# Kernel tuning notes

Measured on AMD Instinct MI355X. Metric: run time of the kernel, lower is better.

## Reference

```python
import jax, jax.numpy as jnp
import numpy as np

B, T, E, HD = 8, 2048, 1024, 64  # batch, seq (== n_ctx), n_embd, head_dim = n_embd // n_head


def setup_inputs() -> dict:
    key = jax.random.key(0)
    k1, k2, k3, k4 = jax.random.split(key, 4)
    x = jax.random.normal(k1, (B, T, E), dtype=jnp.float32)
    s = E ** -0.5  # Linear-like init scale
    Wq = jax.random.normal(k2, (E, HD), dtype=jnp.float32) * s
    Wk = jax.random.normal(k3, (E, HD), dtype=jnp.float32) * s
    Wv = jax.random.normal(k4, (E, HD), dtype=jnp.float32) * s
    return {"x": x, "Wq": Wq, "Wk": Wk, "Wv": Wv}


def reference(x, Wq, Wk, Wv):
    # q,k,v: [B, T, HD]
    q = jnp.einsum('bte,eh->bth', x, Wq)
    k = jnp.einsum('bte,eh->bth', x, Wk)
    v = jnp.einsum('bte,eh->bth', x, Wv)
    scale = k.shape[-1] ** -0.5
    # scores: [B, T, T]
    alpha = jnp.einsum('bqh,bkh->bqk', q, k) * scale
    causal = jnp.tril(jnp.ones((T, T), dtype=bool))
    alpha = jnp.where(causal, alpha, -jnp.inf)
    alpha = jax.nn.softmax(alpha, axis=-1)
    # dropout with p=0.0 is identity in eval
    h = jnp.einsum('bqk,bkh->bqh', alpha, v)  # [B, T, HD]
    return h
```

## Files before the change

### kernel.cpp

```cpp
#include <hip/hip_runtime.h>
#include <hip/hip_bf16.h>
#include <math.h>

#define BATCH 8
#define T 2048
#define E 1024
#define HD 64
#define BT (BATCH * T)

typedef __bf16 bf16_t;
typedef bf16_t bf16x4 __attribute__((ext_vector_type(4)));
typedef bf16_t bf16x8 __attribute__((ext_vector_type(8)));
typedef float f32x4 __attribute__((ext_vector_type(4)));

#define MFMA(a, b, c) __builtin_amdgcn_mfma_f32_16x16x32_bf16((a), (b), (c), 0, 0, 0)

#define QSCALE (0.125f * 1.44269504088896340736f)


__global__ __launch_bounds__(256) void prep_w(const float* __restrict__ Wq,
                                              const float* __restrict__ Wk,
                                              const float* __restrict__ Wv,
                                              bf16_t* __restrict__ WTt) {
    const int nt  = blockIdx.x >> 3;
    const int kc0 = (blockIdx.x & 7) * 128;
    const int tid = threadIdx.x;
    const int l16 = tid & 15;
    const int k8  = (kc0 >> 3) + (tid >> 4);
    const int n   = nt * 16 + l16;
    const int m   = n >> 6;
    const int col = n & 63;
    const float* W = (m == 0) ? Wq : (m == 1) ? Wk : Wv;
    const float scale = (m == 0) ? QSCALE : 1.0f;
    bf16x8 o;
#pragma unroll
    for (int j = 0; j < 8; j++) {
        o[j] = (bf16_t)(W[(size_t)(k8 * 8 + j) * HD + col] * scale);
    }
    *reinterpret_cast<bf16x8*>(WTt + (size_t)nt * 16384 + k8 * 128 + l16 * 8) = o;
}

__global__ __launch_bounds__(512, 2) void qkv_proj(
    const float* __restrict__ x,
    const bf16_t* __restrict__ WTt,
    bf16_t* __restrict__ qt,
    bf16_t* __restrict__ kt,
    bf16_t* __restrict__ vt)
{
    __shared__ __align__(16) bf16_t xb[64][1024];

    const int tid  = threadIdx.x;
    const int lane = tid & 63;
    const int l16  = lane & 15;
    const int quad = lane >> 4;
    const int wc   = (tid >> 6) & 3;
    const int wr   = tid >> 8;
    const int rowbase0 = blockIdx.x * 64;

    {
        const int r   = tid >> 3;
        const int s   = tid & 7;
        const int swz = (r & 7) << 4;
        const float* gsrc = x + (size_t)(rowbase0 + r) * E + s * 128;
        char* drow = reinterpret_cast<char*>(&xb[r][0]);
#pragma unroll
        for (int half = 0; half < 2; half++) {
            f32x4 v[16];
#pragma unroll
            for (int i = 0; i < 16; i++)
                v[i] = *reinterpret_cast<const f32x4*>(gsrc + half * 64 + i * 4);
            __builtin_amdgcn_sched_barrier(0);
#pragma unroll
            for (int j = 0; j < 8; j++) {
                bf16x8 w8;
#pragma unroll
                for (int u = 0; u < 4; u++) {
                    w8[u]     = (bf16_t)v[2 * j][u];
                    w8[4 + u] = (bf16_t)v[2 * j + 1][u];
                }
                const int off = s * 256 + half * 128 + j * 16;
                *reinterpret_cast<bf16x8*>(drow + (off ^ swz)) = w8;
            }
        }
    }
    __syncthreads();

    const bf16_t* Bb = WTt + (size_t)(wc * 3) * 16384 + lane * 8;
    f32x4 acc[2][3] = {};

    for (int kc = 0; kc < E; kc += 64) {
        bf16x8 bf[2][3];
#pragma unroll
        for (int ks = 0; ks < 2; ks++)
#pragma unroll
            for (int tc = 0; tc < 3; tc++)
                bf[ks][tc] = *reinterpret_cast<const bf16x8*>(
                    Bb + (size_t)tc * 16384 + (kc + ks * 32) * 16);

#pragma unroll
        for (int g = 0; g < 2; g++) {
            const int row = wr * 32 + g * 16 + l16;
            const int swz = (row & 7) << 4;
            const char* rbase = reinterpret_cast<const char*>(&xb[row][0]);
            const bf16x8 a0 = *reinterpret_cast<const bf16x8*>(
                rbase + ((kc * 2 + quad * 16) ^ swz));
            const bf16x8 a1 = *reinterpret_cast<const bf16x8*>(
                rbase + ((kc * 2 + 64 + quad * 16) ^ swz));
#pragma unroll
            for (int tc = 0; tc < 3; tc++) acc[g][tc] = MFMA(a0, bf[0][tc], acc[g][tc]);
#pragma unroll
            for (int tc = 0; tc < 3; tc++) acc[g][tc] = MFMA(a1, bf[1][tc], acc[g][tc]);
        }
    }

#pragma unroll
    for (int g = 0; g < 2; g++) {
        const int rowbase = rowbase0 + wr * 32 + g * 16;
#pragma unroll
        for (int tc = 0; tc < 3; tc++) {
            const int n0  = wc * 48 + tc * 16;
            const int m   = n0 >> 6;
            const int tcg = (n0 & 63) >> 4;
            if (m < 2) {
                bf16_t* dst = (m == 0) ? qt : kt;
                const size_t o0 = (size_t)(rowbase >> 4) * 1024 +
                                  (size_t)(tcg * 2 + (l16 >> 3)) * 128 + (l16 & 7);
#pragma unroll
                for (int r = 0; r < 4; r++) {
                    dst[o0 + (quad * 4 + r) * 8] = (bf16_t)acc[g][tc][r];
                }
            } else {
                const int b_    = rowbase >> 11;
                const int tbase = rowbase & (T - 1);
                const size_t o0 = (size_t)b_ * 131072 +
                                  (size_t)((tbase >> 3) + (quad >> 1)) * 128 +
                                  l16 * 8 + (quad & 1) * 4 + (size_t)tcg * 32768;
                bf16x4 pv;
#pragma unroll
                for (int r = 0; r < 4; r++) pv[r] = (bf16_t)acc[g][tc][r];
                *reinterpret_cast<bf16x4*>(vt + o0) = pv;
            }
        }
    }
}

__global__ __launch_bounds__(512, 2) void attn(
    const bf16_t* __restrict__ qtl,
    const bf16_t* __restrict__ ktl,
    const bf16_t* __restrict__ vtl,
    float* __restrict__ out)
{
    __shared__ __align__(16) bf16_t plds[8][16][40];
    __shared__ float opart[8][16][66];
    __shared__ float lpart[8][16];

    const int wave = threadIdx.x >> 6;
    const int lane = threadIdx.x & 63;
    const int l16  = lane & 15;
    const int quad = lane >> 4;
    const int group = wave >> 2;
    const int kw    = wave & 3;

    const int b  = blockIdx.x >> 6;
    const int pr = blockIdx.x & 63;
    const int qt = group ? (127 - pr) : pr;
    const int rowbase = qt * 16;

    const bf16_t* Qb = qtl + (size_t)((b * T + rowbase) >> 4) * 1024 + lane * 8;
    const bf16_t* Kb = ktl + (size_t)b * T * 64 + lane * 8;
    const bf16_t* Vb = vtl + (size_t)b * 131072 + lane * 8;

    const bf16x8 qf0 = *reinterpret_cast<const bf16x8*>(Qb);
    const bf16x8 qf1 = *reinterpret_cast<const bf16x8*>(Qb + 512);

    f32x4 o[4] = {};
    f32x4 lrun = {};

    const int nch = (rowbase + 47) >> 5;

    int k0 = kw * 32;
    bf16x8 kfa0 = *reinterpret_cast<const bf16x8*>(Kb + k0 * 64);
    bf16x8 kfb0 = *reinterpret_cast<const bf16x8*>(Kb + k0 * 64 + 512);
    bf16x8 kfa1 = *reinterpret_cast<const bf16x8*>(Kb + k0 * 64 + 1024);
    bf16x8 kfb1 = *reinterpret_cast<const bf16x8*>(Kb + k0 * 64 + 1536);
    bf16x8 vf0 = *reinterpret_cast<const bf16x8*>(Vb + k0 * 16);
    bf16x8 vf1 = *reinterpret_cast<const bf16x8*>(Vb + k0 * 16 + 32768);
    bf16x8 vf2 = *reinterpret_cast<const bf16x8*>(Vb + k0 * 16 + 65536);
    bf16x8 vf3 = *reinterpret_cast<const bf16x8*>(Vb + k0 * 16 + 98304);

    for (int c = kw; c < nch; c += 4) {
        k0 = c * 32;
        const int cn = (c + 4 < nch) ? (c + 4) : c;
        const int kn = cn * 32;
        bf16x8 nkfa0 = *reinterpret_cast<const bf16x8*>(Kb + kn * 64);
        bf16x8 nkfb0 = *reinterpret_cast<const bf16x8*>(Kb + kn * 64 + 512);
        bf16x8 nkfa1 = *reinterpret_cast<const bf16x8*>(Kb + kn * 64 + 1024);
        bf16x8 nkfb1 = *reinterpret_cast<const bf16x8*>(Kb + kn * 64 + 1536);
        bf16x8 nvf0 = *reinterpret_cast<const bf16x8*>(Vb + kn * 16);
        bf16x8 nvf1 = *reinterpret_cast<const bf16x8*>(Vb + kn * 16 + 32768);
        bf16x8 nvf2 = *reinterpret_cast<const bf16x8*>(Vb + kn * 16 + 65536);
        bf16x8 nvf3 = *reinterpret_cast<const bf16x8*>(Vb + kn * 16 + 98304);

        f32x4 s_lo = {};
        f32x4 s_hi = {};
        s_lo = MFMA(qf0, kfa0, s_lo);
        s_lo = MFMA(qf1, kfb0, s_lo);
        s_hi = MFMA(qf0, kfa1, s_hi);
        s_hi = MFMA(qf1, kfb1, s_hi);

        if (k0 + 31 > rowbase) {
            const int row = rowbase + quad * 4;
#pragma unroll
            for (int r = 0; r < 4; r++) {
                if (k0 + l16 > row + r)      s_lo[r] = -INFINITY;
                if (k0 + 16 + l16 > row + r) s_hi[r] = -INFINITY;
            }
        }

#pragma unroll
        for (int r = 0; r < 4; r++) {
            const float p0 = exp2f(s_lo[r]);
            const float p1 = exp2f(s_hi[r]);
            lrun[r] += p0 + p1;
            plds[wave][quad * 4 + r][l16]      = (bf16_t)p0;
            plds[wave][quad * 4 + r][16 + l16] = (bf16_t)p1;
        }
        const bf16x8 pf = *reinterpret_cast<const bf16x8*>(&plds[wave][l16][quad * 8]);

        o[0] = MFMA(pf, vf0, o[0]);
        o[1] = MFMA(pf, vf1, o[1]);
        o[2] = MFMA(pf, vf2, o[2]);
        o[3] = MFMA(pf, vf3, o[3]);

        kfa0 = nkfa0; kfb0 = nkfb0; kfa1 = nkfa1; kfb1 = nkfb1;
        vf0 = nvf0; vf1 = nvf1; vf2 = nvf2; vf3 = nvf3;
    }

#pragma unroll
    for (int r = 0; r < 4; r++) {
        float l = lrun[r];
        l += __shfl_xor(l, 1);
        l += __shfl_xor(l, 2);
        l += __shfl_xor(l, 4);
        l += __shfl_xor(l, 8);
        if (l16 == 0) lpart[wave][quad * 4 + r] = l;
#pragma unroll
        for (int nb = 0; nb < 4; nb++) {
            opart[wave][quad * 4 + r][nb * 16 + l16] = o[nb][r];
        }
    }
    __syncthreads();

    const int g    = threadIdx.x >> 8;
    const int gtid = threadIdx.x & 255;
    const int qtg  = g ? (127 - pr) : pr;
    const size_t outbase = (size_t)b * T + qtg * 16;
#pragma unroll
    for (int pass = 0; pass < 4; pass++) {
        const int row = pass * 4 + (gtid >> 6);
        const int col = gtid & 63;
        float osum = 0.f, lsum = 0.f;
#pragma unroll
        for (int w = 0; w < 4; w++) {
            osum += opart[g * 4 + w][row][col];
            lsum += lpart[g * 4 + w][row];
        }
        out[(outbase + row) * HD + col] = osum / lsum;
    }
}

extern "C" void kernel_launch(void* const* d_in, const int* in_sizes, int n_in,
                              void* d_out, int out_size, void* d_ws, size_t ws_size,
                              hipStream_t stream) {
    const float* x  = (const float*)d_in[0];
    const float* Wq = (const float*)d_in[1];
    const float* Wk = (const float*)d_in[2];
    const float* Wv = (const float*)d_in[3];
    float* out = (float*)d_out;

    bf16_t* ws  = (bf16_t*)d_ws;
    bf16_t* WTt = ws;
    bf16_t* qtl = WTt + (size_t)192 * E;
    bf16_t* ktl = qtl + (size_t)BT * HD;
    bf16_t* vtl = ktl + (size_t)BT * HD;

    prep_w<<<96, 256, 0, stream>>>(Wq, Wk, Wv, WTt);
    qkv_proj<<<256, 512, 0, stream>>>(x, WTt, qtl, ktl, vtl);
    attn<<<512, 512, 0, stream>>>(qtl, ktl, vtl, out);
}
```

Baseline: 122.9 us.

## Split QKV projection K dimension across wave halves with LDS reduction

The QKV projection kernel now gives each wave all 64 rows and half of the K dimension, rather than half of the rows and all of K. Partial accumulators from the second wave group are reduced through shared memory (reusing the x buffer) before the first group writes output. This halves the weight-fragment global loads per wave relative to MFMA work. The x staging load is also reorganised so a wave's lanes read contiguous 1 KB segments, for more coalesced global reads. In exchange it adds two extra barriers, an LDS partial-sum round trip, and more accumulator registers per wave.

Measured after the change: 119.4 us. -2.9%, faster.

```diff
diff --git a/kernel.cpp b/kernel.cpp
--- a/kernel.cpp
+++ b/kernel.cpp
@@ -50,62 +50,65 @@
     __shared__ __align__(16) bf16_t xb[64][1024];
 
     const int tid  = threadIdx.x;
+    const int w    = tid >> 6;
     const int lane = tid & 63;
     const int l16  = lane & 15;
     const int quad = lane >> 4;
-    const int wc   = (tid >> 6) & 3;
-    const int wr   = tid >> 8;
+    const int wk   = w >> 2;
+    const int wc   = w & 3;
     const int rowbase0 = blockIdx.x * 64;
 
     {
-        const int r   = tid >> 3;
-        const int s   = tid & 7;
-        const int swz = (r & 7) << 4;
-        const float* gsrc = x + (size_t)(rowbase0 + r) * E + s * 128;
-        char* drow = reinterpret_cast<char*>(&xb[r][0]);
-#pragma unroll
-        for (int half = 0; half < 2; half++) {
-            f32x4 v[16];
-#pragma unroll
-            for (int i = 0; i < 16; i++)
-                v[i] = *reinterpret_cast<const f32x4*>(gsrc + half * 64 + i * 4);
+#pragma unroll
+        for (int rd = 0; rd < 4; rd++) {
+            f32x4 v[8];
+#pragma unroll
+            for (int j = 0; j < 8; j++) {
+                const int gi = w * 32 + rd * 8 + j;
+                const int r  = gi >> 2;
+                const int q  = gi & 3;
+                v[j] = *reinterpret_cast<const f32x4*>(
+                    x + (size_t)(rowbase0 + r) * E + q * 256 + lane * 4);
+            }
             __builtin_amdgcn_sched_barrier(0);
 #pragma unroll
             for (int j = 0; j < 8; j++) {
-                bf16x8 w8;
-#pragma unroll
-                for (int u = 0; u < 4; u++) {
-                    w8[u]     = (bf16_t)v[2 * j][u];
-                    w8[4 + u] = (bf16_t)v[2 * j + 1][u];
-                }
-                const int off = s * 256 + half * 128 + j * 16;
-                *reinterpret_cast<bf16x8*>(drow + (off ^ swz)) = w8;
+                const int gi = w * 32 + rd * 8 + j;
+                const int r  = gi >> 2;
+                const int q  = gi & 3;
+                bf16x4 w4;
+#pragma unroll
+                for (int u = 0; u < 4; u++) w4[u] = (bf16_t)v[j][u];
+                char* base = reinterpret_cast<char*>(&xb[r][0]);
+                const int off = (q * 512 + lane * 8) ^ ((r & 7) << 4);
+                *reinterpret_cast<bf16x4*>(base + off) = w4;
             }
         }
     }
     __syncthreads();
 
     const bf16_t* Bb = WTt + (size_t)(wc * 3) * 16384 + lane * 8;
-    f32x4 acc[2][3] = {};
-
-    for (int kc = 0; kc < E; kc += 64) {
+    f32x4 acc[4][3] = {};
+
+    for (int kc8 = 0; kc8 < 8; kc8++) {
+        const int kk = wk * 512 + kc8 * 64;
         bf16x8 bf[2][3];
 #pragma unroll
         for (int ks = 0; ks < 2; ks++)
 #pragma unroll
             for (int tc = 0; tc < 3; tc++)
                 bf[ks][tc] = *reinterpret_cast<const bf16x8*>(
-                    Bb + (size_t)tc * 16384 + (kc + ks * 32) * 16);
-
-#pragma unroll
-        for (int g = 0; g < 2; g++) {
-            const int row = wr * 32 + g * 16 + l16;
+                    Bb + (size_t)tc * 16384 + (kk + ks * 32) * 16);
+
+#pragma unroll
+        for (int g = 0; g < 4; g++) {
+            const int row = g * 16 + l16;
             const int swz = (row & 7) << 4;
-            const char* rbase = reinterpret_cast<const char*>(&xb[row][0]);
+            const char* rb = reinterpret_cast<const char*>(&xb[row][0]);
             const bf16x8 a0 = *reinterpret_cast<const bf16x8*>(
-                rbase + ((kc * 2 + quad * 16) ^ swz));
+                rb + ((kk * 2 + quad * 16) ^ swz));
             const bf16x8 a1 = *reinterpret_cast<const bf16x8*>(
-                rbase + ((kc * 2 + 64 + quad * 16) ^ swz));
+                rb + ((kk * 2 + 64 + quad * 16) ^ swz));
 #pragma unroll
             for (int tc = 0; tc < 3; tc++) acc[g][tc] = MFMA(a0, bf[0][tc], acc[g][tc]);
 #pragma unroll
@@ -113,32 +116,54 @@
         }
     }
 
-#pragma unroll
-    for (int g = 0; g < 2; g++) {
-        const int rowbase = rowbase0 + wr * 32 + g * 16;
-#pragma unroll
-        for (int tc = 0; tc < 3; tc++) {
-            const int n0  = wc * 48 + tc * 16;
-            const int m   = n0 >> 6;
-            const int tcg = (n0 & 63) >> 4;
-            if (m < 2) {
-                bf16_t* dst = (m == 0) ? qt : kt;
-                const size_t o0 = (size_t)(rowbase >> 4) * 1024 +
-                                  (size_t)(tcg * 2 + (l16 >> 3)) * 128 + (l16 & 7);
-#pragma unroll
-                for (int r = 0; r < 4; r++) {
-                    dst[o0 + (quad * 4 + r) * 8] = (bf16_t)acc[g][tc][r];
+    __syncthreads();
+    float* pbuf = reinterpret_cast<float*>(&xb[0][0]);
+    if (wk == 1) {
+#pragma unroll
+        for (int g = 0; g < 4; g++)
+#pragma unroll
+            for (int tc = 0; tc < 3; tc++) {
+                const int idx = (((wc * 4 + g) * 3) + tc) * 256 + lane * 4;
+                *reinterpret_cast<f32x4*>(pbuf + idx) = acc[g][tc];
+            }
+    }
+    __syncthreads();
+    if (wk == 0) {
+#pragma unroll
+        for (int g = 0; g < 4; g++)
+#pragma unroll
+            for (int tc = 0; tc < 3; tc++) {
+                const int idx = (((wc * 4 + g) * 3) + tc) * 256 + lane * 4;
+                acc[g][tc] += *reinterpret_cast<const f32x4*>(pbuf + idx);
+            }
+
+#pragma unroll
+        for (int g = 0; g < 4; g++) {
+            const int rowbase = rowbase0 + g * 16;
+#pragma unroll
+            for (int tc = 0; tc < 3; tc++) {
+                const int n0  = wc * 48 + tc * 16;
+                const int m   = n0 >> 6;
+                const int tcg = (n0 & 63) >> 4;
+                if (m < 2) {
+                    bf16_t* dst = (m == 0) ? qt : kt;
+                    const size_t o0 = (size_t)(rowbase >> 4) * 1024 +
+                                      (size_t)(tcg * 2 + (l16 >> 3)) * 128 + (l16 & 7);
+#pragma unroll
+                    for (int r = 0; r < 4; r++) {
+                        dst[o0 + (quad * 4 + r) * 8] = (bf16_t)acc[g][tc][r];
+                    }
+                } else {
+                    const int b_    = rowbase >> 11;
+                    const int tbase = rowbase & (T - 1);
+                    const size_t o0 = (size_t)b_ * 131072 +
+                                      (size_t)((tbase >> 3) + (quad >> 1)) * 128 +
+                                      l16 * 8 + (quad & 1) * 4 + (size_t)tcg * 32768;
+                    bf16x4 pv;
+#pragma unroll
+                    for (int r = 0; r < 4; r++) pv[r] = (bf16_t)acc[g][tc][r];
+                    *reinterpret_cast<bf16x4*>(vt + o0) = pv;
                 }
-            } else {
-                const int b_    = rowbase >> 11;
-                const int tbase = rowbase & (T - 1);
-                const size_t o0 = (size_t)b_ * 131072 +
-                                  (size_t)((tbase >> 3) + (quad >> 1)) * 128 +
-                                  l16 * 8 + (quad & 1) * 4 + (size_t)tcg * 32768;
-                bf16x4 pv;
-#pragma unroll
-                for (int r = 0; r < 4; r++) pv[r] = (bf16_t)acc[g][tc][r];
-                *reinterpret_cast<bf16x4*>(vt + o0) = pv;
             }
         }
     }
```
